# Optimization experiments

Hardware: AMD Instinct MI355X
Metric: run time of the kernel (lower is better)

## Reference

```python
import jax, jax.numpy as jnp
import numpy as np

SHAPELET_SIZE = 64
NUM_SHAPELETS = 128
IN_CHANNELS = 8


def setup_inputs() -> dict:
    key = jax.random.key(0)
    k1, k2 = jax.random.split(key)
    x = jax.random.normal(k1, (64, IN_CHANNELS, 2048), dtype=jnp.float32)
    shapelets = jax.random.normal(k2, (IN_CHANNELS, NUM_SHAPELETS, SHAPELET_SIZE), dtype=jnp.float32)
    return {"x": x, "shapelets": shapelets}


def _znorm(s):
    # Z-normalize along the time-step axis (dim 2), matching Znormalize_dim(shapelets, 2)
    mu = jnp.mean(s, axis=2, keepdims=True)
    sd = jnp.std(s, axis=2, keepdims=True)
    return (s - mu) / sd


def reference(x, shapelets):
    # x: (N, C, L); shapelets: (C, K, S)
    S = shapelets.shape[-1]
    N, C, L = x.shape
    W = L - S + 1
    # unfold(2, S, 1): sliding windows -> (N, C, W, S)
    idx = jnp.arange(W)[:, None] + jnp.arange(S)[None, :]  # (W, S)
    xw = x[:, :, idx]  # (N, C, W, S)
    sh = _znorm(shapelets)  # (C, K, S)
    # Euclidean cdist via ||a||^2 + ||b||^2 - 2 a.b (avoids (N,C,W,K,S) blowup)
    sq_x = jnp.sum(xw * xw, axis=-1)          # (N, C, W)
    sq_s = jnp.sum(sh * sh, axis=-1)          # (C, K)
    cross = jnp.einsum('ncws,cks->ncwk', xw, sh)  # (N, C, W, K)
    d2 = sq_x[..., None] + sq_s[None, :, None, :] - 2.0 * cross
    d = jnp.sqrt(jnp.maximum(d2, 1e-12))      # (N, C, W, K)
    # sum over channels, then global min over windows -> (N, 1, K)
    dsum = jnp.sum(d, axis=1)                 # (N, W, K)
    out = jnp.min(dsum, axis=1)[:, None, :]   # (N, 1, K)
    return out
```

## Files before the change

kernel.cpp:

```cpp
#include <hip/hip_runtime.h>
#include <math.h>

#define C 8
#define K 128
#define S 64
#define L 2048
#define NB 64
#define W (L - S + 1)
#define TW 128
#define NTW 16
#define XCS 200
#define XFS 200

typedef __attribute__((ext_vector_type(8))) short bf16x8;
typedef __attribute__((ext_vector_type(4))) short short4v;
typedef __attribute__((ext_vector_type(4))) float f32x4;

__device__ __forceinline__ unsigned short f2bf(float f) {
  unsigned int u = __float_as_uint(f);
  u += 0x7FFFu + ((u >> 16) & 1u);
  return (unsigned short)(u >> 16);
}

__global__ __launch_bounds__(256) void prep_kernel(const float* __restrict__ sh,
                                                   unsigned short* __restrict__ shzB,
                                                   float* __restrict__ sqs,
                                                   float* __restrict__ out) {
  int tid = blockIdx.x * 256 + threadIdx.x;
  if (tid < NB * K) out[tid] = __int_as_float(0x7F800000);
  int gid = blockIdx.x * 4 + (threadIdx.x >> 6);
  int lane = threadIdx.x & 63;
  float v = sh[(size_t)gid * S + lane];
  float s1 = v, s2 = v * v;
#pragma unroll
  for (int off = 32; off > 0; off >>= 1) {
    s1 += __shfl_down(s1, off);
    s2 += __shfl_down(s2, off);
  }
  s1 = __shfl(s1, 0);
  s2 = __shfl(s2, 0);
  float mu = s1 * (1.0f / S);
  float sd = sqrtf(fmaxf(s2 * (1.0f / S) - mu * mu, 0.0f));
  float z = (v - mu) / sd;
  int c = gid >> 7, k = gid & (K - 1), s = lane;
  int idx = c * 8192 + ((k >> 4) * 2 + (s >> 5)) * 512 +
            ((((s >> 3) & 3) * 16 + (k & 15)) * 8) + (s & 7);
  shzB[idx] = f2bf(-2.0f * z);
  float z2 = z * z;
#pragma unroll
  for (int off = 32; off > 0; off >>= 1) z2 += __shfl_down(z2, off);
  if (lane == 0) sqs[gid] = z2;
}

__global__ __launch_bounds__(512, 4) void main_kernel(const float* __restrict__ x,
                                                      const unsigned short* __restrict__ shzB,
                                                      const float* __restrict__ sqs,
                                                      int* __restrict__ out) {
  __shared__ __align__(16) unsigned short bbuf[2][8192];
  __shared__ __align__(16) unsigned short xcop[C][4][XCS];
  __shared__ __align__(16) float sqx[C][TW];
  __shared__ __align__(16) float sqsl[C * K];

  const int t = threadIdx.x;
  const int lane = t & 63;
  const int wave = t >> 6;
  const int wgrp = wave & 1;
  const int kgrp = wave >> 1;
  const int col = lane & 15;
  const int quad = lane >> 4;
  const int n = blockIdx.y;
  const int w0 = blockIdx.x * TW;
  const float* xn = x + (size_t)n * C * L;

  {
    const unsigned short* g = shzB + t * 8;
    unsigned short* lb = &bbuf[0][wave * 512];
#pragma unroll
    for (int i = 0; i < 2; ++i)
      __builtin_amdgcn_global_load_lds(
          (const __attribute__((address_space(1))) void*)(g + i * 4096),
          (__attribute__((address_space(3))) void*)(lb + i * 4096), 16, 0, 0);
  }

  float* xf = (float*)&bbuf[1][0];
#pragma unroll
  for (int j = 0; j < 4; ++j) {
    int s = j * 512 + t;
    if (s < C * XFS) {
      int c = s / XFS, e = s - c * XFS;
      int g = w0 + e;
      xf[s] = (e < 192 && g < L) ? xn[c * L + g] : 0.0f;
    }
  }
  sqsl[t] = sqs[t];
  sqsl[t + 512] = sqs[t + 512];
  __syncthreads();

#pragma unroll
  for (int j = 0; j < 6; ++j) {
    int idx = j * 512 + t;
    int c = idx / 384, rem = idx - c * 384;
    int r = rem / 96, i2 = rem - r * 96;
    int i = i2 * 2;
    unsigned int pk = (unsigned int)f2bf(xf[c * XFS + i + r]) |
                      ((unsigned int)f2bf(xf[c * XFS + i + r + 1]) << 16);
    *(unsigned int*)&xcop[c][r][i] = pk;
  }
  {
    int c = wave, wl = lane * 2;
    const float* xr = xf + c * XFS;
    float s0 = 0.0f;
#pragma unroll
    for (int si = 0; si < S; ++si) { float v = xr[wl + si]; s0 = fmaf(v, v, s0); }
    sqx[c][wl] = s0;
    float a = xr[wl + S], b = xr[wl];
    sqx[c][wl + 1] = s0 + a * a - b * b;
  }
  __syncthreads();

  const f32x4 z4 = {0.0f, 0.0f, 0.0f, 0.0f};
  f32x4 dsum[4][2];
#pragma unroll
  for (int a = 0; a < 4; ++a)
#pragma unroll
    for (int b = 0; b < 2; ++b) dsum[a][b] = z4;

  const int r4 = col & 3;
  const int abase = wgrp * 64 + (col - r4) + quad * 8;

  for (int c = 0; c < C; ++c) {
    if (c + 1 < C) {
      const unsigned short* g = shzB + (c + 1) * 8192 + t * 8;
      unsigned short* lb = &bbuf[(c + 1) & 1][wave * 512];
#pragma unroll
      for (int i = 0; i < 2; ++i)
        __builtin_amdgcn_global_load_lds(
            (const __attribute__((address_space(1))) void*)(g + i * 4096),
            (__attribute__((address_space(3))) void*)(lb + i * 4096), 16, 0, 0);
    }
    const unsigned short* bb = bbuf[c & 1];
    const unsigned short* xc = &xcop[c][r4][0];

    bf16x8 bfr[2][2];
#pragma unroll
    for (int ks = 0; ks < 2; ++ks)
#pragma unroll
      for (int kt = 0; kt < 2; ++kt)
        bfr[ks][kt] = *(const bf16x8*)(bb + ((kgrp * 2 + kt) * 2 + ks) * 512 + lane * 8);

    f32x4 acc[4][2];
    float sq0 = sqsl[c * K + kgrp * 32 + col];
    float sq1 = sqsl[c * K + kgrp * 32 + 16 + col];
#pragma unroll
    for (int wt = 0; wt < 4; ++wt) {
      f32x4 sx = *(const f32x4*)&sqx[c][wgrp * 64 + wt * 16 + quad * 4];
#pragma unroll
      for (int i = 0; i < 4; ++i) {
        acc[wt][0][i] = sx[i] + sq0;
        acc[wt][1][i] = sx[i] + sq1;
      }
    }

#pragma unroll
    for (int ks = 0; ks < 2; ++ks) {
      bf16x8 afr[4];
#pragma unroll
      for (int wt = 0; wt < 4; ++wt) {
        int b = abase + wt * 16 + ks * 32;
        short4v lo = *(const short4v*)(xc + b);
        short4v hi = *(const short4v*)(xc + b + 4);
        afr[wt] = __builtin_shufflevector(lo, hi, 0, 1, 2, 3, 4, 5, 6, 7);
      }
#pragma unroll
      for (int wt = 0; wt < 4; ++wt) {
        acc[wt][0] = __builtin_amdgcn_mfma_f32_16x16x32_bf16(afr[wt], bfr[ks][0], acc[wt][0], 0, 0, 0);
        acc[wt][1] = __builtin_amdgcn_mfma_f32_16x16x32_bf16(afr[wt], bfr[ks][1], acc[wt][1], 0, 0, 0);
      }
    }

#pragma unroll
    for (int wt = 0; wt < 4; ++wt)
#pragma unroll
      for (int kt = 0; kt < 2; ++kt)
#pragma unroll
        for (int i = 0; i < 4; ++i)
          dsum[wt][kt][i] += __builtin_amdgcn_sqrtf(fmaxf(acc[wt][kt][i], 1e-12f));

    __syncthreads();
  }

  const float INF = __int_as_float(0x7F800000);
  int wbase = w0 + wgrp * 64;
#pragma unroll
  for (int kt = 0; kt < 2; ++kt) {
    float mv = INF;
#pragma unroll
    for (int wt = 0; wt < 4; ++wt)
#pragma unroll
      for (int i = 0; i < 4; ++i) {
        int w = wbase + wt * 16 + quad * 4 + i;
        mv = (w < W) ? fminf(mv, dsum[wt][kt][i]) : mv;
      }
    mv = fminf(mv, __shfl_xor(mv, 16));
    mv = fminf(mv, __shfl_xor(mv, 32));
    if (quad == 0)
      atomicMin(&out[n * K + kgrp * 32 + kt * 16 + col], __float_as_int(mv));
  }
}

extern "C" void kernel_launch(void* const* d_in, const int* in_sizes, int n_in,
                              void* d_out, int out_size, void* d_ws, size_t ws_size,
                              hipStream_t stream) {
  const float* x = (const float*)d_in[0];
  const float* sh = (const float*)d_in[1];
  float* out = (float*)d_out;
  unsigned short* shzB = (unsigned short*)d_ws;
  float* sqs = (float*)((char*)d_ws + C * K * S * 2);

  prep_kernel<<<256, 256, 0, stream>>>(sh, shzB, sqs, out);
  main_kernel<<<dim3(NTW, NB), 512, 0, stream>>>(x, shzB, sqs, (int*)out);
}
```

Before: 96.56 us.

## Switch to 32x32x16 MFMA tiles with 256-thread blocks and relaid shapelet layout

Replaces the 16x16x32 bf16 MFMA tiling with 32x32x16 MFMAs. Each of four waves now covers 64 windows by 64 shapelets, and the prep kernel writes shapelets in a matching new B-fragment layout. The block shrinks from 512 to 256 threads, the shapelet prefetch is moved after the x staging so the staging buffer can be reused, and packing uses the hardware bf16x2 conversion. The aim is fewer MFMA issues and fragment loads per unit of work, at the cost of more accumulator registers per thread and lower occupancy.

```diff
diff --git a/kernel.cpp b/kernel.cpp
--- a/kernel.cpp
+++ b/kernel.cpp
@@ -1,4 +1,5 @@
 #include <hip/hip_runtime.h>
+#include <hip/hip_bf16.h>
 #include <math.h>
 
 #define C 8
@@ -15,11 +16,22 @@
 typedef __attribute__((ext_vector_type(8))) short bf16x8;
 typedef __attribute__((ext_vector_type(4))) short short4v;
 typedef __attribute__((ext_vector_type(4))) float f32x4;
+typedef __attribute__((ext_vector_type(16))) float f32x16;
 
 __device__ __forceinline__ unsigned short f2bf(float f) {
   unsigned int u = __float_as_uint(f);
   u += 0x7FFFu + ((u >> 16) & 1u);
   return (unsigned short)(u >> 16);
+}
+
+__device__ __forceinline__ unsigned int pkbf(float a, float b) {
+  __hip_bfloat162 h = __float22bfloat162_rn(make_float2(a, b));
+  return *reinterpret_cast<unsigned int*>(&h);
+}
+
+__device__ __forceinline__ void gll16(const void* g, void* l) {
+  __builtin_amdgcn_global_load_lds((const __attribute__((address_space(1))) void*)g,
+                                   (__attribute__((address_space(3))) void*)l, 16, 0, 0);
 }
 
 __global__ __launch_bounds__(256) void prep_kernel(const float* __restrict__ sh,
@@ -43,8 +55,8 @@
   float sd = sqrtf(fmaxf(s2 * (1.0f / S) - mu * mu, 0.0f));
   float z = (v - mu) / sd;
   int c = gid >> 7, k = gid & (K - 1), s = lane;
-  int idx = c * 8192 + ((k >> 4) * 2 + (s >> 5)) * 512 +
-            ((((s >> 3) & 3) * 16 + (k & 15)) * 8) + (s & 7);
+  int idx = c * 8192 + (k >> 5) * 2048 + (s >> 4) * 512 +
+            ((((s >> 3) & 1) * 32 + (k & 31)) * 8) + (s & 7);
   shzB[idx] = f2bf(-2.0f * z);
   float z2 = z * z;
 #pragma unroll
@@ -52,7 +64,7 @@
   if (lane == 0) sqs[gid] = z2;
 }
 
-__global__ __launch_bounds__(512, 4) void main_kernel(const float* __restrict__ x,
+__global__ __launch_bounds__(256, 3) void main_kernel(const float* __restrict__ x,
                                                       const unsigned short* __restrict__ shzB,
                                                       const float* __restrict__ sqs,
                                                       int* __restrict__ out) {
@@ -66,26 +78,16 @@
   const int wave = t >> 6;
   const int wgrp = wave & 1;
   const int kgrp = wave >> 1;
-  const int col = lane & 15;
-  const int quad = lane >> 4;
+  const int m = lane & 31;
+  const int h = lane >> 5;
   const int n = blockIdx.y;
   const int w0 = blockIdx.x * TW;
   const float* xn = x + (size_t)n * C * L;
 
-  {
-    const unsigned short* g = shzB + t * 8;
-    unsigned short* lb = &bbuf[0][wave * 512];
-#pragma unroll
-    for (int i = 0; i < 2; ++i)
-      __builtin_amdgcn_global_load_lds(
-          (const __attribute__((address_space(1))) void*)(g + i * 4096),
-          (__attribute__((address_space(3))) void*)(lb + i * 4096), 16, 0, 0);
-  }
-
-  float* xf = (float*)&bbuf[1][0];
-#pragma unroll
-  for (int j = 0; j < 4; ++j) {
-    int s = j * 512 + t;
+  float* xf = (float*)&bbuf[0][0];
+#pragma unroll
+  for (int j = 0; j < 7; ++j) {
+    int s = j * 256 + t;
     if (s < C * XFS) {
       int c = s / XFS, e = s - c * XFS;
       int g = w0 + e;
@@ -93,118 +95,122 @@
     }
   }
   sqsl[t] = sqs[t];
+  sqsl[t + 256] = sqs[t + 256];
   sqsl[t + 512] = sqs[t + 512];
+  sqsl[t + 768] = sqs[t + 768];
   __syncthreads();
 
 #pragma unroll
-  for (int j = 0; j < 6; ++j) {
-    int idx = j * 512 + t;
+  for (int j = 0; j < 12; ++j) {
+    int idx = j * 256 + t;
     int c = idx / 384, rem = idx - c * 384;
     int r = rem / 96, i2 = rem - r * 96;
     int i = i2 * 2;
-    unsigned int pk = (unsigned int)f2bf(xf[c * XFS + i + r]) |
-                      ((unsigned int)f2bf(xf[c * XFS + i + r + 1]) << 16);
-    *(unsigned int*)&xcop[c][r][i] = pk;
+    *(unsigned int*)&xcop[c][r][i] = pkbf(xf[c * XFS + i + r], xf[c * XFS + i + r + 1]);
   }
   {
-    int c = wave, wl = lane * 2;
+    int c = t >> 5, wl = (t & 31) * 4;
     const float* xr = xf + c * XFS;
-    float s0 = 0.0f;
-#pragma unroll
-    for (int si = 0; si < S; ++si) { float v = xr[wl + si]; s0 = fmaf(v, v, s0); }
+    float p0 = 0.f, p1 = 0.f, p2 = 0.f, p3 = 0.f;
+#pragma unroll
+    for (int si = 0; si < S; si += 4) {
+      float v0 = xr[wl + si], v1 = xr[wl + si + 1], v2 = xr[wl + si + 2], v3 = xr[wl + si + 3];
+      p0 = fmaf(v0, v0, p0); p1 = fmaf(v1, v1, p1);
+      p2 = fmaf(v2, v2, p2); p3 = fmaf(v3, v3, p3);
+    }
+    float s0 = (p0 + p1) + (p2 + p3);
     sqx[c][wl] = s0;
-    float a = xr[wl + S], b = xr[wl];
-    sqx[c][wl + 1] = s0 + a * a - b * b;
+#pragma unroll
+    for (int q = 1; q < 4; ++q) {
+      float a = xr[wl + S - 1 + q], b = xr[wl + q - 1];
+      s0 += a * a - b * b;
+      sqx[c][wl + q] = s0;
+    }
   }
   __syncthreads();
 
-  const f32x4 z4 = {0.0f, 0.0f, 0.0f, 0.0f};
-  f32x4 dsum[4][2];
-#pragma unroll
-  for (int a = 0; a < 4; ++a)
-#pragma unroll
-    for (int b = 0; b < 2; ++b) dsum[a][b] = z4;
-
-  const int r4 = col & 3;
-  const int abase = wgrp * 64 + (col - r4) + quad * 8;
+#pragma unroll
+  for (int i = 0; i < 4; ++i)
+    gll16(shzB + i * 2048 + t * 8, &bbuf[0][i * 2048 + wave * 512]);
+
+  f32x16 dsum[2][2];
+#pragma unroll
+  for (int a = 0; a < 2; ++a)
+#pragma unroll
+    for (int b = 0; b < 2; ++b)
+#pragma unroll
+      for (int e = 0; e < 16; ++e) dsum[a][b][e] = 0.0f;
+
+  const int r4 = m & 3;
 
   for (int c = 0; c < C; ++c) {
+    __syncthreads();
     if (c + 1 < C) {
-      const unsigned short* g = shzB + (c + 1) * 8192 + t * 8;
-      unsigned short* lb = &bbuf[(c + 1) & 1][wave * 512];
-#pragma unroll
-      for (int i = 0; i < 2; ++i)
-        __builtin_amdgcn_global_load_lds(
-            (const __attribute__((address_space(1))) void*)(g + i * 4096),
-            (__attribute__((address_space(3))) void*)(lb + i * 4096), 16, 0, 0);
+#pragma unroll
+      for (int i = 0; i < 4; ++i)
+        gll16(shzB + (c + 1) * 8192 + i * 2048 + t * 8,
+              &bbuf[(c + 1) & 1][i * 2048 + wave * 512]);
     }
     const unsigned short* bb = bbuf[c & 1];
-    const unsigned short* xc = &xcop[c][r4][0];
-
-    bf16x8 bfr[2][2];
-#pragma unroll
-    for (int ks = 0; ks < 2; ++ks)
-#pragma unroll
-      for (int kt = 0; kt < 2; ++kt)
-        bfr[ks][kt] = *(const bf16x8*)(bb + ((kgrp * 2 + kt) * 2 + ks) * 512 + lane * 8);
-
-    f32x4 acc[4][2];
-    float sq0 = sqsl[c * K + kgrp * 32 + col];
-    float sq1 = sqsl[c * K + kgrp * 32 + 16 + col];
-#pragma unroll
-    for (int wt = 0; wt < 4; ++wt) {
-      f32x4 sx = *(const f32x4*)&sqx[c][wgrp * 64 + wt * 16 + quad * 4];
-#pragma unroll
-      for (int i = 0; i < 4; ++i) {
-        acc[wt][0][i] = sx[i] + sq0;
-        acc[wt][1][i] = sx[i] + sq1;
+
+    bf16x8 bfr[8];
+#pragma unroll
+    for (int kt = 0; kt < 2; ++kt)
+#pragma unroll
+      for (int ks = 0; ks < 4; ++ks)
+        bfr[kt * 4 + ks] = *(const bf16x8*)(bb + (kgrp * 2 + kt) * 2048 + ks * 512 + lane * 8);
+
+    float sqv0 = sqsl[c * K + kgrp * 64 + m];
+    float sqv1 = sqsl[c * K + kgrp * 64 + 32 + m];
+
+#pragma unroll
+    for (int wsub = 0; wsub < 2; ++wsub) {
+      const int wb = wgrp * 64 + wsub * 32;
+      f32x4 sxv[4];
+#pragma unroll
+      for (int g = 0; g < 4; ++g)
+        sxv[g] = *(const f32x4*)&sqx[c][wb + 8 * g + 4 * h];
+      const unsigned short* xc = &xcop[c][r4][0];
+      bf16x8 af[4];
+#pragma unroll
+      for (int ks = 0; ks < 4; ++ks) {
+        int base = wb + (m - r4) + ks * 16 + 8 * h;
+        short4v lo = *(const short4v*)(xc + base);
+        short4v hi = *(const short4v*)(xc + base + 4);
+        af[ks] = __builtin_shufflevector(lo, hi, 0, 1, 2, 3, 4, 5, 6, 7);
       }
-    }
-
-#pragma unroll
-    for (int ks = 0; ks < 2; ++ks) {
-      bf16x8 afr[4];
-#pragma unroll
-      for (int wt = 0; wt < 4; ++wt) {
-        int b = abase + wt * 16 + ks * 32;
-        short4v lo = *(const short4v*)(xc + b);
-        short4v hi = *(const short4v*)(xc + b + 4);
-        afr[wt] = __builtin_shufflevector(lo, hi, 0, 1, 2, 3, 4, 5, 6, 7);
+#pragma unroll
+      for (int kt = 0; kt < 2; ++kt) {
+        f32x16 acc;
+        float sq = kt ? sqv1 : sqv0;
+#pragma unroll
+        for (int g = 0; g < 4; ++g)
+#pragma unroll
+          for (int i = 0; i < 4; ++i) acc[g * 4 + i] = sxv[g][i] + sq;
+#pragma unroll
+        for (int ks = 0; ks < 4; ++ks)
+          acc = __builtin_amdgcn_mfma_f32_32x32x16_bf16(af[ks], bfr[kt * 4 + ks], acc, 0, 0, 0);
+#pragma unroll
+        for (int e = 0; e < 16; ++e)
+          dsum[wsub][kt][e] += __builtin_amdgcn_sqrtf(fmaxf(acc[e], 0.0f));
       }
-#pragma unroll
-      for (int wt = 0; wt < 4; ++wt) {
-        acc[wt][0] = __builtin_amdgcn_mfma_f32_16x16x32_bf16(afr[wt], bfr[ks][0], acc[wt][0], 0, 0, 0);
-        acc[wt][1] = __builtin_amdgcn_mfma_f32_16x16x32_bf16(afr[wt], bfr[ks][1], acc[wt][1], 0, 0, 0);
-      }
-    }
-
-#pragma unroll
-    for (int wt = 0; wt < 4; ++wt)
-#pragma unroll
-      for (int kt = 0; kt < 2; ++kt)
-#pragma unroll
-        for (int i = 0; i < 4; ++i)
-          dsum[wt][kt][i] += __builtin_amdgcn_sqrtf(fmaxf(acc[wt][kt][i], 1e-12f));
-
-    __syncthreads();
+    }
   }
 
   const float INF = __int_as_float(0x7F800000);
-  int wbase = w0 + wgrp * 64;
 #pragma unroll
   for (int kt = 0; kt < 2; ++kt) {
     float mv = INF;
 #pragma unroll
-    for (int wt = 0; wt < 4; ++wt)
-#pragma unroll
-      for (int i = 0; i < 4; ++i) {
-        int w = wbase + wt * 16 + quad * 4 + i;
-        mv = (w < W) ? fminf(mv, dsum[wt][kt][i]) : mv;
+    for (int wsub = 0; wsub < 2; ++wsub)
+#pragma unroll
+      for (int e = 0; e < 16; ++e) {
+        int w = w0 + wgrp * 64 + wsub * 32 + (e & 3) + 8 * (e >> 2) + 4 * h;
+        mv = (w < W) ? fminf(mv, dsum[wsub][kt][e]) : mv;
       }
-    mv = fminf(mv, __shfl_xor(mv, 16));
     mv = fminf(mv, __shfl_xor(mv, 32));
-    if (quad == 0)
-      atomicMin(&out[n * K + kgrp * 32 + kt * 16 + col], __float_as_int(mv));
+    if (h == 0)
+      atomicMin(&out[n * K + kgrp * 64 + kt * 32 + m], __float_as_int(mv));
   }
 }
 
@@ -218,5 +224,5 @@
   float* sqs = (float*)((char*)d_ws + C * K * S * 2);
 
   prep_kernel<<<256, 256, 0, stream>>>(sh, shzB, sqs, out);
-  main_kernel<<<dim3(NTW, NB), 512, 0, stream>>>(x, shzB, sqs, (int*)out);
-}
+  main_kernel<<<dim3(NTW, NB), 256, 0, stream>>>(x, shzB, sqs, (int*)out);
+}
```

New measurement: 98.76 us. +2.3%, slower.
